# Kernel tuning notes

Measured on AMD Instinct MI355X. Metric: run time of the kernel, lower is better.

## Reference

```python
import jax, jax.numpy as jnp
import numpy as np

TAU = 0.07
EPS = 1e-12  # matches torch F.normalize default eps


def setup_inputs() -> dict:
    key = jax.random.key(0)
    k1, k2 = jax.random.split(key)
    B, C, H, W, K = 4, 256, 256, 256, 19
    feat = jax.random.normal(k1, (B, C, H, W), dtype=jnp.float32)
    # binary ground-truth one-hot-ish masks; gt.eq(1) selects positives
    gt = jax.random.randint(k2, (B, K, H, W), 0, 2).astype(jnp.float32)
    return {"feat": feat, "gt": gt}


def _l2norm(x, axis):
    n = jnp.sqrt(jnp.sum(x * x, axis=axis, keepdims=True))
    return x / jnp.maximum(n, EPS)


def reference(feat, gt):
    # feat: [B,C,H,W], gt: [B,K,H,W] binary
    pos = (gt == 1.0).astype(feat.dtype)              # [B,K,H,W]
    fnorm = _l2norm(feat, axis=1)                     # per-pixel L2 normalize over C
    # scatter-add normalized features into class prototypes
    k0 = jnp.einsum('bkhw,bchw->kc', pos, fnorm)      # [K,C]
    k0n = _l2norm(k0, axis=1)                         # [K,C]
    # prototype-vs-pixel similarities, softmax over classes
    logits = jnp.einsum('kc,bchw->bkhw', k0n, fnorm) / TAU  # [B,K,H,W]
    logp = jax.nn.log_softmax(logits, axis=1)
    num_pos = jnp.sum(pos)
    loss = -jnp.sum(pos * logp) / num_pos
    return loss
```

## Files before the change

kernel.cpp:

```cpp
#include <hip/hip_runtime.h>
#include <math.h>

namespace {
constexpr int Cn = 256;
constexpr int Kn = 19;
constexpr int HW = 256 * 256;
constexpr int P  = 4 * HW;
constexpr float TAUv = 0.07f;
constexpr float EPSv = 1e-12f;

constexpr int K0_OFF   = 0;
constexpr int K0N_OFF  = 4864;
constexpr int SUMS_OFF = 9728;
constexpr int ZERO_N   = 9730;
constexpr int P1_GRID  = 1024;
constexpr int P3_GRID  = P / 256;
}

__device__ __forceinline__ float bcast_f(float x) {
  return __uint_as_float((unsigned)__builtin_amdgcn_readfirstlane((int)__float_as_uint(x)));
}
__device__ __forceinline__ unsigned bcast_u(unsigned x) {
  return (unsigned)__builtin_amdgcn_readfirstlane((int)x);
}

__global__ __launch_bounds__(256) void gc_init(float* __restrict__ ws) {
  int i = blockIdx.x * 256 + threadIdx.x;
  if (i < ZERO_N) ws[i] = 0.0f;
}

__global__ __launch_bounds__(256, 4) void gc_phase1(const float* __restrict__ feat,
                                                    const float* __restrict__ gt,
                                                    float* __restrict__ k0) {
  __shared__ float tile[32 * 256];
  __shared__ float part[256];
  __shared__ float rnL[32];
  __shared__ unsigned mskL[32];

  const int t = threadIdx.x;
  const int p = t & 31;
  const int g = t >> 5;

  float acc[Kn];
#pragma unroll
  for (int k = 0; k < Kn; k++) acc[k] = 0.0f;

  for (int tid = blockIdx.x; tid < P / 32; tid += gridDim.x) {
    const int p0  = tid << 5;
    const int b   = p0 >> 16;
    const int hw0 = p0 & (HW - 1);
    const float* fb = feat + (size_t)b * (Cn * HW) + hw0;

    __syncthreads();

    float v[32];
#pragma unroll
    for (int j = 0; j < 32; j++) v[j] = fb[(size_t)((g << 5) + j) * HW + p];
    float ss = 0.0f;
#pragma unroll
    for (int j = 0; j < 32; j++) {
      const int c = (g << 5) + j;
      ss += v[j] * v[j];
      tile[(p << 8) + (c ^ p)] = v[j];
    }
    part[t] = ss;

    unsigned msk = 0;
    if (t < 32) {
      const float* gb = gt + (size_t)b * (Kn * HW) + hw0 + p;
#pragma unroll
      for (int k = 0; k < Kn; k++)
        msk |= (gb[(size_t)k * HW] == 1.0f) ? (1u << k) : 0u;
    }

    __syncthreads();

    if (t < 32) {
      float fss = 0.0f;
#pragma unroll
      for (int q = 0; q < 8; q++) fss += part[(q << 5) + p];
      rnL[p]  = 1.0f / fmaxf(sqrtf(fss), EPSv);
      mskL[p] = msk;
    }

    __syncthreads();

#pragma unroll 8
    for (int pp = 0; pp < 32; pp++) {
      const float    rn = bcast_f(rnL[pp]);
      const unsigned mk = bcast_u(mskL[pp]);
      const float    fv = tile[(pp << 8) + (t ^ pp)];
#pragma unroll
      for (int k = 0; k < Kn; k++) {
        const float w = ((mk >> k) & 1u) ? rn : 0.0f;
        acc[k] = fmaf(fv, w, acc[k]);
      }
    }
  }

#pragma unroll
  for (int k = 0; k < Kn; k++) atomicAdd(&k0[k * 256 + t], acc[k]);
}

__global__ __launch_bounds__(256) void gc_phase2(const float* __restrict__ k0,
                                                 float* __restrict__ k0n) {
  const int lane = threadIdx.x & 63;
  const int wv   = threadIdx.x >> 6;
  for (int r = wv; r < Kn; r += 4) {
    float s = 0.0f;
#pragma unroll
    for (int j = 0; j < 4; j++) {
      const float v = k0[r * 256 + (j << 6) + lane];
      s += v * v;
    }
#pragma unroll
    for (int off = 32; off > 0; off >>= 1) s += __shfl_down(s, off);
    s = __shfl(s, 0);
    const float rn = 1.0f / fmaxf(sqrtf(s), EPSv);
#pragma unroll
    for (int j = 0; j < 4; j++) {
      const int c = (j << 6) + lane;
      k0n[r * 256 + c] = k0[r * 256 + c] * rn;
    }
  }
}

__device__ __forceinline__ void p3_load(float (&dst)[16],
                                        const float* __restrict__ fb, int base) {
#pragma unroll
  for (int j = 0; j < 16; j++) dst[j] = fb[(size_t)(base + j) * HW];
}

__device__ __forceinline__ void p3_compute(const float (&v)[16], int c0,
                                           const float* __restrict__ k0n,
                                           float (&dot)[Kn], float& ss) {
#pragma unroll
  for (int j4 = 0; j4 < 16; j4 += 4) {
    const float f0 = v[j4 + 0], f1 = v[j4 + 1];
    const float f2 = v[j4 + 2], f3 = v[j4 + 3];
    ss = fmaf(f0, f0, ss); ss = fmaf(f1, f1, ss);
    ss = fmaf(f2, f2, ss); ss = fmaf(f3, f3, ss);
#pragma unroll
    for (int k = 0; k < Kn; k++) {
      const float4 w = *(const float4*)(k0n + k * 256 + c0 + j4);
      dot[k] = fmaf(f3, w.w, fmaf(f2, w.z, fmaf(f1, w.y, fmaf(f0, w.x, dot[k]))));
    }
  }
}

__global__ __launch_bounds__(256, 4) void gc_phase3(const float* __restrict__ feat,
                                                    const float* __restrict__ gt,
                                                    const float* __restrict__ k0n,
                                                    float* __restrict__ sums) {
  const int t    = threadIdx.x;
  const int pix0 = blockIdx.x << 8;
  const int b    = pix0 >> 16;
  const int hw   = (pix0 & (HW - 1)) + t;
  const float* fb = feat + (size_t)b * (Cn * HW) + hw;

  float dot[Kn];
#pragma unroll
  for (int k = 0; k < Kn; k++) dot[k] = 0.0f;
  float ss = 0.0f;

  float va[16], vb[16];
  p3_load(va, fb, 0);
  for (int c0 = 0; c0 < Cn; c0 += 32) {
    p3_load(vb, fb, c0 + 16);
    p3_compute(va, c0, k0n, dot, ss);
    if (c0 + 32 < Cn) p3_load(va, fb, c0 + 32);
    p3_compute(vb, c0 + 16, k0n, dot, ss);
  }

  const float sc = 1.0f / (fmaxf(sqrtf(ss), EPSv) * TAUv);
  float mx = -1e30f;
#pragma unroll
  for (int k = 0; k < Kn; k++) { dot[k] *= sc; mx = fmaxf(mx, dot[k]); }
  float se = 0.0f;
#pragma unroll
  for (int k = 0; k < Kn; k++) se += __expf(dot[k] - mx);
  const float lse = __logf(se) + mx;

  const float* gb = gt + (size_t)b * (Kn * HW) + hw;
  float lsum = 0.0f, npos = 0.0f;
#pragma unroll
  for (int k = 0; k < Kn; k++) {
    if (gb[(size_t)k * HW] == 1.0f) { lsum += lse - dot[k]; npos += 1.0f; }
  }

#pragma unroll
  for (int off = 32; off > 0; off >>= 1) {
    lsum += __shfl_down(lsum, off);
    npos += __shfl_down(npos, off);
  }
  if ((t & 63) == 0) {
    atomicAdd(&sums[0], lsum);
    atomicAdd(&sums[1], npos);
  }
}

__global__ void gc_finalize(const float* __restrict__ sums, float* __restrict__ out) {
  if (threadIdx.x == 0 && blockIdx.x == 0)
    out[0] = sums[0] / sums[1];
}

extern "C" void kernel_launch(void* const* d_in, const int* in_sizes, int n_in,
                              void* d_out, int out_size, void* d_ws, size_t ws_size,
                              hipStream_t stream) {
  const float* feat = (const float*)d_in[0];
  const float* gt   = (const float*)d_in[1];
  float* ws  = (float*)d_ws;
  float* out = (float*)d_out;

  float* k0   = ws + K0_OFF;
  float* k0n  = ws + K0N_OFF;
  float* sums = ws + SUMS_OFF;

  gc_init<<<dim3((ZERO_N + 255) / 256), dim3(256), 0, stream>>>(ws);
  gc_phase1<<<dim3(P1_GRID), dim3(256), 0, stream>>>(feat, gt, k0);
  gc_phase2<<<dim3(1), dim3(256), 0, stream>>>(k0, k0n);
  gc_phase3<<<dim3(P3_GRID), dim3(256), 0, stream>>>(feat, gt, k0n, sums);
  gc_finalize<<<dim3(1), dim3(64), 0, stream>>>(sums, out);
}
```

Before: 634.0 us.

## Vectorize feature loads with float4 and compute four pixels per thread

Phase 1 now loads features as float4 (four adjacent pixels per thread) and reduces the squared norms through a padded 32x33 shared array. Phase 3 processes four pixels per thread with 128-thread blocks, so each k0n float4 load is reused across four pixels and the gt mask is read as float4. The aim is fewer, wider global loads and less redundant prototype traffic. The cost is a large rise in register use (76 dot accumulators plus 16 float4 buffers), which may cut occupancy or cause spills.

```diff
diff --git a/kernel.cpp b/kernel.cpp
--- a/kernel.cpp
+++ b/kernel.cpp
@@ -14,7 +14,7 @@
 constexpr int SUMS_OFF = 9728;
 constexpr int ZERO_N   = 9730;
 constexpr int P1_GRID  = 1024;
-constexpr int P3_GRID  = P / 256;
+constexpr int P3_GRID  = P / 512;
 }
 
 __device__ __forceinline__ float bcast_f(float x) {
@@ -33,13 +33,13 @@
                                                     const float* __restrict__ gt,
                                                     float* __restrict__ k0) {
   __shared__ float tile[32 * 256];
-  __shared__ float part[256];
+  __shared__ float part2[32][33];
   __shared__ float rnL[32];
   __shared__ unsigned mskL[32];
 
-  const int t = threadIdx.x;
-  const int p = t & 31;
-  const int g = t >> 5;
+  const int t  = threadIdx.x;
+  const int pq = t & 7;
+  const int g  = t >> 3;
 
   float acc[Kn];
 #pragma unroll
@@ -53,21 +53,33 @@
 
     __syncthreads();
 
-    float v[32];
-#pragma unroll
-    for (int j = 0; j < 32; j++) v[j] = fb[(size_t)((g << 5) + j) * HW + p];
-    float ss = 0.0f;
-#pragma unroll
-    for (int j = 0; j < 32; j++) {
-      const int c = (g << 5) + j;
-      ss += v[j] * v[j];
-      tile[(p << 8) + (c ^ p)] = v[j];
-    }
-    part[t] = ss;
+    float4 v4[8];
+#pragma unroll
+    for (int j = 0; j < 8; j++)
+      v4[j] = *(const float4*)&fb[(size_t)((g << 3) + j) * HW + (pq << 2)];
+
+    float ps0 = 0.f, ps1 = 0.f, ps2 = 0.f, ps3 = 0.f;
+#pragma unroll
+    for (int j = 0; j < 8; j++) {
+      const int c  = (g << 3) + j;
+      const int px = pq << 2;
+      ps0 = fmaf(v4[j].x, v4[j].x, ps0);
+      ps1 = fmaf(v4[j].y, v4[j].y, ps1);
+      ps2 = fmaf(v4[j].z, v4[j].z, ps2);
+      ps3 = fmaf(v4[j].w, v4[j].w, ps3);
+      tile[((px + 0) << 8) + (c ^ (px + 0))] = v4[j].x;
+      tile[((px + 1) << 8) + (c ^ (px + 1))] = v4[j].y;
+      tile[((px + 2) << 8) + (c ^ (px + 2))] = v4[j].z;
+      tile[((px + 3) << 8) + (c ^ (px + 3))] = v4[j].w;
+    }
+    part2[(pq << 2) + 0][g] = ps0;
+    part2[(pq << 2) + 1][g] = ps1;
+    part2[(pq << 2) + 2][g] = ps2;
+    part2[(pq << 2) + 3][g] = ps3;
 
     unsigned msk = 0;
     if (t < 32) {
-      const float* gb = gt + (size_t)b * (Kn * HW) + hw0 + p;
+      const float* gb = gt + (size_t)b * (Kn * HW) + hw0 + t;
 #pragma unroll
       for (int k = 0; k < Kn; k++)
         msk |= (gb[(size_t)k * HW] == 1.0f) ? (1u << k) : 0u;
@@ -78,9 +90,9 @@
     if (t < 32) {
       float fss = 0.0f;
 #pragma unroll
-      for (int q = 0; q < 8; q++) fss += part[(q << 5) + p];
-      rnL[p]  = 1.0f / fmaxf(sqrtf(fss), EPSv);
-      mskL[p] = msk;
+      for (int gg = 0; gg < 32; gg++) fss += part2[t][gg];
+      rnL[t]  = 1.0f / fmaxf(sqrtf(fss), EPSv);
+      mskL[t] = msk;
     }
 
     __syncthreads();
@@ -125,67 +137,87 @@
   }
 }
 
-__device__ __forceinline__ void p3_load(float (&dst)[16],
-                                        const float* __restrict__ fb, int base) {
-#pragma unroll
-  for (int j = 0; j < 16; j++) dst[j] = fb[(size_t)(base + j) * HW];
-}
-
-__device__ __forceinline__ void p3_compute(const float (&v)[16], int c0,
-                                           const float* __restrict__ k0n,
-                                           float (&dot)[Kn], float& ss) {
-#pragma unroll
-  for (int j4 = 0; j4 < 16; j4 += 4) {
-    const float f0 = v[j4 + 0], f1 = v[j4 + 1];
-    const float f2 = v[j4 + 2], f3 = v[j4 + 3];
-    ss = fmaf(f0, f0, ss); ss = fmaf(f1, f1, ss);
-    ss = fmaf(f2, f2, ss); ss = fmaf(f3, f3, ss);
+__device__ __forceinline__ void p3_load4(float4 (&dst)[8],
+                                         const float* __restrict__ fb, int base) {
+#pragma unroll
+  for (int j = 0; j < 8; j++)
+    dst[j] = *(const float4*)&fb[(size_t)(base + j) * HW];
+}
+
+__device__ __forceinline__ void p3_compute4(const float4 (&v)[8], int c0,
+                                            const float* __restrict__ k0n,
+                                            float (&dot)[Kn][4], float (&ss)[4]) {
+#pragma unroll
+  for (int j4 = 0; j4 < 8; j4 += 4) {
+    const float4 f0 = v[j4 + 0], f1 = v[j4 + 1];
+    const float4 f2 = v[j4 + 2], f3 = v[j4 + 3];
+    ss[0] = fmaf(f0.x, f0.x, ss[0]); ss[0] = fmaf(f1.x, f1.x, ss[0]);
+    ss[0] = fmaf(f2.x, f2.x, ss[0]); ss[0] = fmaf(f3.x, f3.x, ss[0]);
+    ss[1] = fmaf(f0.y, f0.y, ss[1]); ss[1] = fmaf(f1.y, f1.y, ss[1]);
+    ss[1] = fmaf(f2.y, f2.y, ss[1]); ss[1] = fmaf(f3.y, f3.y, ss[1]);
+    ss[2] = fmaf(f0.z, f0.z, ss[2]); ss[2] = fmaf(f1.z, f1.z, ss[2]);
+    ss[2] = fmaf(f2.z, f2.z, ss[2]); ss[2] = fmaf(f3.z, f3.z, ss[2]);
+    ss[3] = fmaf(f0.w, f0.w, ss[3]); ss[3] = fmaf(f1.w, f1.w, ss[3]);
+    ss[3] = fmaf(f2.w, f2.w, ss[3]); ss[3] = fmaf(f3.w, f3.w, ss[3]);
 #pragma unroll
     for (int k = 0; k < Kn; k++) {
       const float4 w = *(const float4*)(k0n + k * 256 + c0 + j4);
-      dot[k] = fmaf(f3, w.w, fmaf(f2, w.z, fmaf(f1, w.y, fmaf(f0, w.x, dot[k]))));
-    }
-  }
-}
-
-__global__ __launch_bounds__(256, 4) void gc_phase3(const float* __restrict__ feat,
+      dot[k][0] = fmaf(f3.x, w.w, fmaf(f2.x, w.z, fmaf(f1.x, w.y, fmaf(f0.x, w.x, dot[k][0]))));
+      dot[k][1] = fmaf(f3.y, w.w, fmaf(f2.y, w.z, fmaf(f1.y, w.y, fmaf(f0.y, w.x, dot[k][1]))));
+      dot[k][2] = fmaf(f3.z, w.w, fmaf(f2.z, w.z, fmaf(f1.z, w.y, fmaf(f0.z, w.x, dot[k][2]))));
+      dot[k][3] = fmaf(f3.w, w.w, fmaf(f2.w, w.z, fmaf(f1.w, w.y, fmaf(f0.w, w.x, dot[k][3]))));
+    }
+  }
+}
+
+__global__ __launch_bounds__(128, 2) void gc_phase3(const float* __restrict__ feat,
                                                     const float* __restrict__ gt,
                                                     const float* __restrict__ k0n,
                                                     float* __restrict__ sums) {
   const int t    = threadIdx.x;
-  const int pix0 = blockIdx.x << 8;
+  const int pix0 = blockIdx.x << 9;
   const int b    = pix0 >> 16;
-  const int hw   = (pix0 & (HW - 1)) + t;
+  const int hw   = (pix0 & (HW - 1)) + (t << 2);
   const float* fb = feat + (size_t)b * (Cn * HW) + hw;
 
-  float dot[Kn];
-#pragma unroll
-  for (int k = 0; k < Kn; k++) dot[k] = 0.0f;
-  float ss = 0.0f;
-
-  float va[16], vb[16];
-  p3_load(va, fb, 0);
-  for (int c0 = 0; c0 < Cn; c0 += 32) {
-    p3_load(vb, fb, c0 + 16);
-    p3_compute(va, c0, k0n, dot, ss);
-    if (c0 + 32 < Cn) p3_load(va, fb, c0 + 32);
-    p3_compute(vb, c0 + 16, k0n, dot, ss);
-  }
-
-  const float sc = 1.0f / (fmaxf(sqrtf(ss), EPSv) * TAUv);
-  float mx = -1e30f;
-#pragma unroll
-  for (int k = 0; k < Kn; k++) { dot[k] *= sc; mx = fmaxf(mx, dot[k]); }
-  float se = 0.0f;
-#pragma unroll
-  for (int k = 0; k < Kn; k++) se += __expf(dot[k] - mx);
-  const float lse = __logf(se) + mx;
+  float dot[Kn][4];
+#pragma unroll
+  for (int k = 0; k < Kn; k++)
+#pragma unroll
+    for (int i = 0; i < 4; i++) dot[k][i] = 0.0f;
+  float ss[4] = {0.f, 0.f, 0.f, 0.f};
+
+  float4 va[8], vb[8];
+  p3_load4(va, fb, 0);
+  for (int c0 = 0; c0 < Cn; c0 += 16) {
+    p3_load4(vb, fb, c0 + 8);
+    p3_compute4(va, c0, k0n, dot, ss);
+    if (c0 + 16 < Cn) p3_load4(va, fb, c0 + 16);
+    p3_compute4(vb, c0 + 8, k0n, dot, ss);
+  }
 
   const float* gb = gt + (size_t)b * (Kn * HW) + hw;
+  float4 gv[Kn];
+#pragma unroll
+  for (int k = 0; k < Kn; k++) gv[k] = *(const float4*)&gb[(size_t)k * HW];
+
   float lsum = 0.0f, npos = 0.0f;
 #pragma unroll
-  for (int k = 0; k < Kn; k++) {
-    if (gb[(size_t)k * HW] == 1.0f) { lsum += lse - dot[k]; npos += 1.0f; }
+  for (int i = 0; i < 4; i++) {
+    const float sc = 1.0f / (fmaxf(sqrtf(ss[i]), EPSv) * TAUv);
+    float mx = -1e30f;
+    float d[Kn];
+#pragma unroll
+    for (int k = 0; k < Kn; k++) { d[k] = dot[k][i] * sc; mx = fmaxf(mx, d[k]); }
+    float se = 0.0f;
+#pragma unroll
+    for (int k = 0; k < Kn; k++) se += __expf(d[k] - mx);
+    const float lse = __logf(se) + mx;
+#pragma unroll
+    for (int k = 0; k < Kn; k++) {
+      const float gvi = (i == 0) ? gv[k].x : (i == 1) ? gv[k].y : (i == 2) ? gv[k].z : gv[k].w;
+      if (gvi == 1.0f) { lsum += lse - d[k]; npos += 1.0f; }
+    }
   }
 
 #pragma unroll
@@ -219,6 +251,6 @@
   gc_init<<<dim3((ZERO_N + 255) / 256), dim3(256), 0, stream>>>(ws);
   gc_phase1<<<dim3(P1_GRID), dim3(256), 0, stream>>>(feat, gt, k0);
   gc_phase2<<<dim3(1), dim3(256), 0, stream>>>(k0, k0n);
-  gc_phase3<<<dim3(P3_GRID), dim3(256), 0, stream>>>(feat, gt, k0n, sums);
+  gc_phase3<<<dim3(P3_GRID), dim3(128), 0, stream>>>(feat, gt, k0n, sums);
   gc_finalize<<<dim3(1), dim3(64), 0, stream>>>(sums, out);
 }
```

Result: faster. 549.4 us (-13.3%).
